# Kernel tuning notes

Hardware: AMD Instinct MI355X
Metric: run time of the kernel (lower is better)

Reference implementation:

```python
import jax, jax.numpy as jnp
import numpy as np

EPS = 1e-6


def rms_norm(h, w):
    # T5-style: no mean subtraction, no bias; variance in fp32
    var = jnp.mean(jnp.square(h.astype(jnp.float32)), axis=-1, keepdims=True)
    h = h * jax.lax.rsqrt(var + EPS)
    return w * h


def split_heads(t, n_heads):
    b, n, d = t.shape
    return t.reshape(b, n, n_heads, d // n_heads).transpose(0, 2, 1, 3)  # [B,H,N,dk]


def unify_heads(t):
    b, h, n, dk = t.shape
    return t.transpose(0, 2, 1, 3).reshape(b, n, h * dk)


def attention(q_in, kv_in, bias, wq, wk, wv, wo, n_heads):
    q = split_heads(q_in @ wq, n_heads)   # [B,H,Nq,dk]
    k = split_heads(kv_in @ wk, n_heads)  # [B,H,Nk,dk]
    v = split_heads(kv_in @ wv, n_heads)
    scores = jnp.einsum('bhqd,bhkd->bhqk', q, k) + bias  # no 1/sqrt(dk) scaling (T5 style)
    w = jax.nn.softmax(scores.astype(jnp.float32), axis=-1).astype(scores.dtype)
    out = jnp.einsum('bhqk,bhkd->bhqd', w, v)
    return unify_heads(out) @ wo


def setup_inputs() -> dict:
    key = jax.random.key(0)
    ks = jax.random.split(key, 18)
    B, N, ENC_N, D, H, DFF = 4, 2048, 1024, 1024, 16, 4096
    s = 0.02
    inp = {
        'x': jax.random.normal(ks[0], (B, N, D), jnp.float32),
        'encoding': jax.random.normal(ks[1], (B, ENC_N, D), jnp.float32),
        'self_attention_position_bias': jax.random.normal(ks[2], (1, H, 1, N), jnp.float32),
        'enc_dec_attention_position_bias': jax.random.normal(ks[3], (1, H, N, ENC_N), jnp.float32),
        'wq_s': jax.random.normal(ks[4], (D, D), jnp.float32) * s,
        'wk_s': jax.random.normal(ks[5], (D, D), jnp.float32) * s,
        'wv_s': jax.random.normal(ks[6], (D, D), jnp.float32) * s,
        'wo_s': jax.random.normal(ks[7], (D, D), jnp.float32) * s,
        'wq_c': jax.random.normal(ks[8], (D, D), jnp.float32) * s,
        'wk_c': jax.random.normal(ks[9], (D, D), jnp.float32) * s,
        'wv_c': jax.random.normal(ks[10], (D, D), jnp.float32) * s,
        'wo_c': jax.random.normal(ks[11], (D, D), jnp.float32) * s,
        'ff1_w': jax.random.normal(ks[12], (D, DFF), jnp.float32) * s,
        'ff2_w': jax.random.normal(ks[13], (DFF, D), jnp.float32) * s,
        'norm1_w': jnp.ones((D,), jnp.float32),
        'norm2_w': jnp.ones((D,), jnp.float32),
        'norm3_w': jnp.ones((D,), jnp.float32),
    }
    return inp


def reference(x, encoding, self_attention_position_bias, enc_dec_attention_position_bias,
              wq_s, wk_s, wv_s, wo_s, wq_c, wk_c, wv_c, wo_c,
              ff1_w, ff2_w, norm1_w, norm2_w, norm3_w):
    n_heads = 16
    # --- self-attention (decoder: single query = last token) ---
    normed = rms_norm(x, norm1_w)
    q_in = normed[:, -1:, :]  # [B,1,D]
    attn_out = attention(q_in, normed, self_attention_position_bias,
                         wq_s, wk_s, wv_s, wo_s, n_heads)  # [B,1,D]
    x = x + attn_out  # broadcast over sequence, matching torch in-place broadcast
    # --- cross-attention ---
    normed = rms_norm(x, norm2_w)
    cross_out = attention(normed, encoding, enc_dec_attention_position_bias,
                          wq_c, wk_c, wv_c, wo_c, n_heads)  # [B,N,D]
    x = x + cross_out
    # --- MLP ---
    normed = rms_norm(x, norm3_w)
    mlp_out = jax.nn.relu(normed @ ff1_w) @ ff2_w
    return x + mlp_out
```

## Files before the change

### kernel.cpp

```cpp
#include <hip/hip_runtime.h>
#include <stdint.h>

typedef unsigned short bfu;
typedef __bf16 bf8v __attribute__((ext_vector_type(8)));
typedef unsigned short us8 __attribute__((ext_vector_type(8)));
typedef unsigned short us4 __attribute__((ext_vector_type(4)));
typedef float f4v __attribute__((ext_vector_type(4)));

__device__ __forceinline__ float bf2f(bfu u) {
    union { unsigned u; float f; } c; c.u = ((unsigned)u) << 16; return c.f;
}
__device__ __forceinline__ bfu f2bf(float f) {
    union { float f; unsigned u; } c; c.f = f;
    unsigned r = c.u + 0x7fffu + ((c.u >> 16) & 1u);
    return (bfu)(r >> 16);
}
__device__ __forceinline__ f4v mfma16(us8 a, us8 b, f4v c) {
    return __builtin_amdgcn_mfma_f32_16x16x32_bf16(
        __builtin_bit_cast(bf8v, a), __builtin_bit_cast(bf8v, b), c, 0, 0, 0);
}

template<int BM, int BN, int EPI>
__global__ __launch_bounds__(256) void gemm_bt(
    const bfu* __restrict__ A, const bfu* __restrict__ Bt,
    const float* __restrict__ resF, void* __restrict__ outP,
    int K, int lda, int ldb, int ldc,
    long long aZs, long long aBs, long long aHs,
    long long bZs, long long bBs, long long bHs,
    long long cZs, long long cBs, long long cHs,
    int bh0)
{
    constexpr int BK = 64;
    constexpr int WM = BM / 2, WN = BN / 2;
    constexpr int TM = WM / 16, TN = WN / 16;
    __shared__ __align__(16) bfu sA[BM * BK];
    __shared__ __align__(16) bfu sB[BN * BK];

    const int tid  = threadIdx.x;
    const int lane = tid & 63;
    const int wid  = tid >> 6;
    const int wr = wid >> 1, wc = wid & 1;

    const int z  = blockIdx.z;
    const int bh = bh0 + z;
    const int bb = bh >> 4, hh = bh & 15;
    const long long aOff = aZs * z + aBs * bb + aHs * hh;
    const long long bOff = bZs * z + bBs * bb + bHs * hh;
    const long long cOff = cZs * z + cBs * bb + cHs * hh;

    const int m0 = blockIdx.y * BM;
    const int n0 = blockIdx.x * BN;

    f4v acc[TM][TN];
    #pragma unroll
    for (int i = 0; i < TM; ++i)
        #pragma unroll
        for (int j = 0; j < TN; ++j)
            acc[i][j] = (f4v)0.0f;

    const bfu* gA = A + aOff + (long long)m0 * lda;
    const bfu* gB = Bt + bOff + (long long)n0 * ldb;
    const int rsub = tid >> 3;
    const int kb   = (tid & 7) * 8;

    for (int k0 = 0; k0 < K; k0 += BK) {
        us8 ra[BM / 32], rb[BN / 32];
        #pragma unroll
        for (int it = 0; it < BM / 32; ++it)
            ra[it] = *(const us8*)(gA + (long long)(it * 32 + rsub) * lda + k0 + kb);
        #pragma unroll
        for (int it = 0; it < BN / 32; ++it)
            rb[it] = *(const us8*)(gB + (long long)(it * 32 + rsub) * ldb + k0 + kb);

        __syncthreads();
        #pragma unroll
        for (int it = 0; it < BM / 32; ++it)
            *(us8*)&sA[(it * 32 + rsub) * BK + kb] = ra[it];
        #pragma unroll
        for (int it = 0; it < BN / 32; ++it)
            *(us8*)&sB[(it * 32 + rsub) * BK + kb] = rb[it];
        __syncthreads();

        #pragma unroll
        for (int kk = 0; kk < BK; kk += 32) {
            const int kro = kk + ((lane >> 4) << 3);
            us8 af[TM], bfr[TN];
            #pragma unroll
            for (int i = 0; i < TM; ++i)
                af[i] = *(const us8*)&sA[(wr * WM + i * 16 + (lane & 15)) * BK + kro];
            #pragma unroll
            for (int j = 0; j < TN; ++j)
                bfr[j] = *(const us8*)&sB[(wc * WN + j * 16 + (lane & 15)) * BK + kro];
            #pragma unroll
            for (int i = 0; i < TM; ++i)
                #pragma unroll
                for (int j = 0; j < TN; ++j)
                    acc[i][j] = mfma16(af[i], bfr[j], acc[i][j]);
        }
    }

    const int quad = lane >> 4;
    const int cn = lane & 15;
    #pragma unroll
    for (int i = 0; i < TM; ++i) {
        #pragma unroll
        for (int j = 0; j < TN; ++j) {
            const int col = n0 + wc * WN + j * 16 + cn;
            #pragma unroll
            for (int r = 0; r < 4; ++r) {
                const int row = m0 + wr * WM + i * 16 + quad * 4 + r;
                const long long idx = cOff + (long long)row * ldc + col;
                const float v = acc[i][j][r];
                if constexpr (EPI == 0) ((bfu*)outP)[idx] = f2bf(v);
                else if constexpr (EPI == 1) ((float*)outP)[idx] = resF[idx] + v;
                else ((bfu*)outP)[idx] = f2bf(fmaxf(v, 0.0f));
            }
        }
    }
}

#define SROW 1032
__global__ __launch_bounds__(256) void xattn(
    const bfu* __restrict__ q2,
    const bfu* __restrict__ k2,
    const bfu* __restrict__ v2t,
    const float* __restrict__ bias,
    bfu* __restrict__ O)
{
    __shared__ __align__(16) bfu S[32 * SROW];
    const int tid = threadIdx.x, lane = tid & 63, wid = tid >> 6;
    const int quad = lane >> 4, l16 = lane & 15;
    const int bh = blockIdx.y, b = bh >> 4, h = bh & 15;
    const int q0 = blockIdx.x * 32;

    const int prow = (wid & 1) * 16;
    const int kh0  = (wid >> 1) * 512;
    const bfu* qbase = q2 + ((long long)b * 2048 + q0 + prow) * 1024 + h * 64;
    const us8 af0 = *(const us8*)(qbase + (long long)l16 * 1024 + quad * 8);
    const us8 af1 = *(const us8*)(qbase + (long long)l16 * 1024 + 32 + quad * 8);
    const bfu* kbase = k2 + (long long)b * 1048576 + h * 64;
    #pragma unroll 4
    for (int t = 0; t < 32; ++t) {
        const int n0 = kh0 + t * 16;
        const bfu* kr = kbase + (long long)(n0 + l16) * 1024 + quad * 8;
        const us8 bf0 = *(const us8*)kr;
        const us8 bf1 = *(const us8*)(kr + 32);
        f4v acc = (f4v)0.0f;
        acc = mfma16(af0, bf0, acc);
        acc = mfma16(af1, bf1, acc);
        #pragma unroll
        for (int r = 0; r < 4; ++r)
            S[(prow + quad * 4 + r) * SROW + n0 + l16] = f2bf(acc[r]);
    }
    __syncthreads();

    const float* bb0 = bias + ((long long)h * 2048 + q0) * 1024;
    for (int rr = 0; rr < 8; ++rr) {
        const int row = wid * 8 + rr;
        bfu* sp = &S[row * SROW + lane * 16];
        const us8 s0 = *(const us8*)sp;
        const us8 s1 = *(const us8*)(sp + 8);
        const float* bp = bb0 + (long long)row * 1024 + lane * 16;
        f4v bv[4];
        #pragma unroll
        for (int j = 0; j < 4; ++j) bv[j] = *(const f4v*)(bp + j * 4);
        float v[16];
        #pragma unroll
        for (int j = 0; j < 8; ++j) v[j] = bf2f(s0[j]) + bv[j >> 2][j & 3];
        #pragma unroll
        for (int j = 0; j < 8; ++j) v[8 + j] = bf2f(s1[j]) + bv[2 + (j >> 2)][j & 3];
        float m = v[0];
        #pragma unroll
        for (int j = 1; j < 16; ++j) m = fmaxf(m, v[j]);
        #pragma unroll
        for (int o = 32; o; o >>= 1) m = fmaxf(m, __shfl_xor(m, o));
        float s = 0.f;
        #pragma unroll
        for (int j = 0; j < 16; ++j) { v[j] = __expf(v[j] - m); s += v[j]; }
        #pragma unroll
        for (int o = 32; o; o >>= 1) s += __shfl_xor(s, o);
        const float inv = 1.0f / s;
        us8 o0, o1;
        #pragma unroll
        for (int j = 0; j < 8; ++j) { o0[j] = f2bf(v[j] * inv); o1[j] = f2bf(v[8 + j] * inv); }
        *(us8*)sp = o0;
        *(us8*)(sp + 8) = o1;
    }
    __syncthreads();

    const int dc0 = (wid >> 1) * 32;
    const bfu* vb = v2t + (long long)bh * 65536;
    f4v acc[2];
    acc[0] = (f4v)0.0f; acc[1] = (f4v)0.0f;
    #pragma unroll 4
    for (int k0 = 0; k0 < 1024; k0 += 32) {
        const us8 pa = *(const us8*)&S[(prow + l16) * SROW + k0 + quad * 8];
        #pragma unroll
        for (int j = 0; j < 2; ++j) {
            const us8 vf = *(const us8*)(vb + (long long)(dc0 + j * 16 + l16) * 1024 + k0 + quad * 8);
            acc[j] = mfma16(pa, vf, acc[j]);
        }
    }
    bfu* ob = O + ((long long)b * 2048 + q0 + prow) * 1024 + h * 64 + dc0;
    #pragma unroll
    for (int j = 0; j < 2; ++j)
        #pragma unroll
        for (int r = 0; r < 4; ++r)
            ob[(long long)(quad * 4 + r) * 1024 + j * 16 + l16] = f2bf(acc[j][r]);
}

__global__ __launch_bounds__(256) void cvt_f2b(
    const float* __restrict__ in, bfu* __restrict__ out)
{
    const long long i = ((long long)blockIdx.x * 256 + threadIdx.x) * 4;
    f4v v = *(const f4v*)(in + i);
    us4 o;
    #pragma unroll
    for (int k = 0; k < 4; ++k) o[k] = f2bf(v[k]);
    *(us4*)(out + i) = o;
}

__global__ __launch_bounds__(256) void transpose_plain(
    const float* __restrict__ in, bfu* __restrict__ out, int R, int C)
{
    __shared__ bfu t[32][33];
    const int r0 = blockIdx.y * 32, c0 = blockIdx.x * 32;
    const int tx = threadIdx.x, ty = threadIdx.y;
    #pragma unroll
    for (int i = 0; i < 32; i += 8)
        t[ty + i][tx] = f2bf(in[(long long)(r0 + ty + i) * C + c0 + tx]);
    __syncthreads();
    #pragma unroll
    for (int i = 0; i < 32; i += 8)
        out[(long long)(c0 + ty + i) * R + r0 + tx] = t[tx][ty + i];
}

__global__ __launch_bounds__(256) void transpose_w8(
    const float* p0, const float* p1, const float* p2, const float* p3,
    const float* p4, const float* p5, const float* p6, const float* p7,
    bfu* __restrict__ out)
{
    __shared__ bfu t[32][33];
    const float* srcs[8] = {p0, p1, p2, p3, p4, p5, p6, p7};
    const int zz = blockIdx.z;
    const float* in = srcs[zz];
    bfu* o = out + (long long)zz * 1048576;
    const int r0 = blockIdx.y * 32, c0 = blockIdx.x * 32;
    const int tx = threadIdx.x, ty = threadIdx.y;
    #pragma unroll
    for (int i = 0; i < 32; i += 8)
        t[ty + i][tx] = f2bf(in[(long long)(r0 + ty + i) * 1024 + c0 + tx]);
    __syncthreads();
    #pragma unroll
    for (int i = 0; i < 32; i += 8)
        o[(long long)(c0 + ty + i) * 1024 + r0 + tx] = t[tx][ty + i];
}

__global__ __launch_bounds__(256) void transpose_v2(
    const bfu* __restrict__ v2, bfu* __restrict__ v2t)
{
    __shared__ bfu t[32][33];
    const int z = blockIdx.z, b = z >> 4, h = z & 15;
    const bfu* in = v2 + (long long)b * 1048576 + h * 64;
    bfu* o = v2t + (long long)z * 65536;
    const int c0 = blockIdx.x * 32, r0 = blockIdx.y * 32;
    const int tx = threadIdx.x, ty = threadIdx.y;
    #pragma unroll
    for (int i = 0; i < 32; i += 8)
        t[ty + i][tx] = in[(long long)(r0 + ty + i) * 1024 + c0 + tx];
    __syncthreads();
    #pragma unroll
    for (int i = 0; i < 32; i += 8)
        o[(long long)(c0 + ty + i) * 1024 + r0 + tx] = t[tx][ty + i];
}

__device__ __forceinline__ float blockSum4(float v, float* red) {
    const int lane = threadIdx.x & 63, wid = threadIdx.x >> 6;
    #pragma unroll
    for (int o = 32; o; o >>= 1) v += __shfl_xor(v, o);
    if (lane == 0) red[wid] = v;
    __syncthreads();
    return red[0] + red[1] + red[2] + red[3];
}

__global__ __launch_bounds__(256) void rmsnorm_f32k(
    const float* __restrict__ X, const float* __restrict__ w, bfu* __restrict__ O)
{
    __shared__ float red[4];
    const long long row = blockIdx.x;
    const int tid = threadIdx.x;
    f4v xv = *(const f4v*)(X + row * 1024 + tid * 4);
    float ss = 0.f;
    #pragma unroll
    for (int i = 0; i < 4; ++i) ss += xv[i] * xv[i];
    ss = blockSum4(ss, red);
    const float sc = rsqrtf(ss * (1.0f / 1024.0f) + 1e-6f);
    f4v wv = *(const f4v*)(w + tid * 4);
    us4 o4;
    #pragma unroll
    for (int i = 0; i < 4; ++i) o4[i] = f2bf(xv[i] * sc * wv[i]);
    *(us4*)(O + row * 1024 + tid * 4) = o4;
}

__global__ __launch_bounds__(256) void add_bcast_rmsnorm(
    const float* __restrict__ X, const float* __restrict__ attn,
    const float* __restrict__ w, float* __restrict__ X1, bfu* __restrict__ O)
{
    __shared__ float red[4];
    const long long row = blockIdx.x;
    const int b = (int)(row >> 11);
    const int tid = threadIdx.x;
    f4v xv = *(const f4v*)(X + row * 1024 + tid * 4);
    f4v av = *(const f4v*)(attn + b * 1024 + tid * 4);
    f4v v;
    float ss = 0.f;
    #pragma unroll
    for (int i = 0; i < 4; ++i) { v[i] = xv[i] + av[i]; ss += v[i] * v[i]; }
    *(f4v*)(X1 + row * 1024 + tid * 4) = v;
    ss = blockSum4(ss, red);
    const float sc = rsqrtf(ss * (1.0f / 1024.0f) + 1e-6f);
    f4v wv = *(const f4v*)(w + tid * 4);
    us4 o4;
    #pragma unroll
    for (int i = 0; i < 4; ++i) o4[i] = f2bf(v[i] * sc * wv[i]);
    *(us4*)(O + row * 1024 + tid * 4) = o4;
}

template<int OUTF>
__global__ __launch_bounds__(256) void vecmat(
    const bfu* __restrict__ A, const bfu* __restrict__ Bt, void* __restrict__ out,
    int K, int N, long long aStride, long long aBase)
{
    __shared__ float sa[1024];
    const int tid = threadIdx.x;
    const int b = blockIdx.y;
    const bfu* ar = A + aBase + (long long)b * aStride;
    for (int k = tid; k < K; k += 256) sa[k] = bf2f(ar[k]);
    __syncthreads();
    const int n = blockIdx.x * 256 + tid;
    if (n < N) {
        const bfu* wr = Bt + (long long)n * K;
        float s = 0.f;
        for (int k = 0; k < K; k += 8) {
            us8 wv = *(const us8*)(wr + k);
            #pragma unroll
            for (int j = 0; j < 8; ++j) s += sa[k + j] * bf2f(wv[j]);
        }
        if constexpr (OUTF) ((float*)out)[(long long)b * N + n] = s;
        else ((bfu*)out)[(long long)b * N + n] = f2bf(s);
    }
}

__global__ __launch_bounds__(256) void decode_attn(
    const bfu* __restrict__ qs, const bfu* __restrict__ Kt,
    const bfu* __restrict__ Vt, const float* __restrict__ bias,
    bfu* __restrict__ osmall)
{
    const int bh = blockIdx.x, b = bh >> 4, h = bh & 15;
    const int tid = threadIdx.x, lane = tid & 63, wid = tid >> 6;
    __shared__ float sq[64];
    __shared__ float sc[2048];
    __shared__ float red[4];
    __shared__ float po[4][64];
    if (tid < 64) sq[tid] = bf2f(qs[b * 1024 + h * 64 + tid]);
    __syncthreads();

    const bfu* Kb = Kt + (long long)b * 2048 * 1024 + h * 64;
    float lmax = -1e30f;
    for (int k = tid; k < 2048; k += 256) {
        const us8* kr = (const us8*)(Kb + (long long)k * 1024);
        float s = 0.f;
        #pragma unroll
        for (int j = 0; j < 8; ++j) {
            us8 kv = kr[j];
            #pragma unroll
            for (int t = 0; t < 8; ++t) s += sq[j * 8 + t] * bf2f(kv[t]);
        }
        s += bias[h * 2048 + k];
        sc[k] = s;
        lmax = fmaxf(lmax, s);
    }
    #pragma unroll
    for (int o = 32; o; o >>= 1) lmax = fmaxf(lmax, __shfl_xor(lmax, o));
    if (lane == 0) red[wid] = lmax;
    __syncthreads();
    const float m = fmaxf(fmaxf(red[0], red[1]), fmaxf(red[2], red[3]));
    __syncthreads();

    float lsum = 0.f;
    for (int k = tid; k < 2048; k += 256) {
        const float e = __expf(sc[k] - m);
        sc[k] = e; lsum += e;
    }
    #pragma unroll
    for (int o = 32; o; o >>= 1) lsum += __shfl_xor(lsum, o);
    if (lane == 0) red[wid] = lsum;
    __syncthreads();
    const float S = red[0] + red[1] + red[2] + red[3];

    const bfu* Vb = Vt + (long long)b * 2048 * 1024 + h * 64;
    const int d = tid & 63, ks = tid >> 6;
    float a = 0.f;
    for (int k = ks * 512; k < ks * 512 + 512; ++k)
        a += sc[k] * bf2f(Vb[(long long)k * 1024 + d]);
    po[ks][d] = a;
    __syncthreads();
    if (tid < 64) {
        const float r = (po[0][tid] + po[1][tid] + po[2][tid] + po[3][tid]) / S;
        osmall[b * 1024 + h * 64 + tid] = f2bf(r);
    }
}

extern "C" void kernel_launch(void* const* d_in, const int* in_sizes, int n_in,
                              void* d_out, int out_size, void* d_ws, size_t ws_size,
                              hipStream_t stream) {
    (void)in_sizes; (void)n_in; (void)out_size; (void)ws_size;
    const float* x     = (const float*)d_in[0];
    const float* enc   = (const float*)d_in[1];
    const float* sbias = (const float*)d_in[2];
    const float* cbias = (const float*)d_in[3];
    const float* wq_s  = (const float*)d_in[4];
    const float* wk_s  = (const float*)d_in[5];
    const float* wv_s  = (const float*)d_in[6];
    const float* wo_s  = (const float*)d_in[7];
    const float* wq_c  = (const float*)d_in[8];
    const float* wk_c  = (const float*)d_in[9];
    const float* wv_c  = (const float*)d_in[10];
    const float* wo_c  = (const float*)d_in[11];
    const float* ff1   = (const float*)d_in[12];
    const float* ff2   = (const float*)d_in[13];
    const float* n1w   = (const float*)d_in[14];
    const float* n2w   = (const float*)d_in[15];
    const float* n3w   = (const float*)d_in[16];
    float* out = (float*)d_out;

    char* ws = (char*)d_ws;
    size_t off = 0;
    auto alloc = [&](size_t bytes) -> void* {
        void* p = (void*)(ws + off);
        off += (bytes + 255) & ~(size_t)255;
        return p;
    };
    bfu*   normed = (bfu*)alloc((size_t)8192 * 1024 * 2);
    bfu*   bufA   = (bfu*)alloc((size_t)8192 * 1024 * 2);
    bfu*   bufB   = (bfu*)alloc((size_t)8192 * 1024 * 2);
    bfu*   k2b    = (bfu*)alloc((size_t)4096 * 1024 * 2);
    bfu*   v2b    = (bfu*)alloc((size_t)4096 * 1024 * 2);
    bfu*   v2t    = (bfu*)alloc((size_t)4096 * 1024 * 2);
    bfu*   encb   = (bfu*)alloc((size_t)4096 * 1024 * 2);
    float* x1f    = (float*)alloc((size_t)8192 * 1024 * 4);
    bfu*   wT     = (bfu*)alloc((size_t)8 * 1048576 * 2);
    bfu*   ff1T   = (bfu*)alloc((size_t)4096 * 1024 * 2);
    bfu*   ff2T   = (bfu*)alloc((size_t)4096 * 1024 * 2);
    bfu*   qsb    = (bfu*)alloc(4 * 1024 * 2);
    bfu*   osm    = (bfu*)alloc(4 * 1024 * 2);
    float* attnv  = (float*)alloc(4 * 1024 * 4);
    bfu*   H1     = bufA;

    const dim3 tb32(32, 8);

    cvt_f2b<<<dim3(4096), 256, 0, stream>>>(enc, encb);
    transpose_w8<<<dim3(32, 32, 8), tb32, 0, stream>>>(
        wq_s, wk_s, wv_s, wo_s, wq_c, wk_c, wv_c, wo_c, wT);
    transpose_plain<<<dim3(128, 32, 1), tb32, 0, stream>>>(ff1, ff1T, 1024, 4096);
    transpose_plain<<<dim3(32, 128, 1), tb32, 0, stream>>>(ff2, ff2T, 4096, 1024);

    rmsnorm_f32k<<<dim3(8192), 256, 0, stream>>>(x, n1w, normed);

    gemm_bt<128, 128, 0><<<dim3(8, 64, 1), 256, 0, stream>>>(
        normed, wT + 1 * 1048576, nullptr, bufA, 1024, 1024, 1024, 1024,
        0, 0, 0, 0, 0, 0, 0, 0, 0, 0);
    gemm_bt<128, 128, 0><<<dim3(8, 64, 1), 256, 0, stream>>>(
        normed, wT + 2 * 1048576, nullptr, bufB, 1024, 1024, 1024, 1024,
        0, 0, 0, 0, 0, 0, 0, 0, 0, 0);
    vecmat<0><<<dim3(4, 4), 256, 0, stream>>>(normed, wT + 0 * 1048576, qsb,
        1024, 1024, (long long)2048 * 1024, (long long)2047 * 1024);
    decode_attn<<<dim3(64), 256, 0, stream>>>(qsb, bufA, bufB, sbias, osm);
    vecmat<1><<<dim3(4, 4), 256, 0, stream>>>(osm, wT + 3 * 1048576, attnv,
        1024, 1024, 1024, 0);
    add_bcast_rmsnorm<<<dim3(8192), 256, 0, stream>>>(x, attnv, n2w, x1f, normed);

    gemm_bt<128, 128, 0><<<dim3(8, 64, 1), 256, 0, stream>>>(
        normed, wT + 4 * 1048576, nullptr, bufA, 1024, 1024, 1024, 1024,
        0, 0, 0, 0, 0, 0, 0, 0, 0, 0);
    gemm_bt<128, 128, 0><<<dim3(8, 32, 1), 256, 0, stream>>>(
        encb, wT + 5 * 1048576, nullptr, k2b, 1024, 1024, 1024, 1024,
        0, 0, 0, 0, 0, 0, 0, 0, 0, 0);
    gemm_bt<128, 128, 0><<<dim3(8, 32, 1), 256, 0, stream>>>(
        encb, wT + 6 * 1048576, nullptr, v2b, 1024, 1024, 1024, 1024,
        0, 0, 0, 0, 0, 0, 0, 0, 0, 0);
    transpose_v2<<<dim3(2, 32, 64), tb32, 0, stream>>>(v2b, v2t);

    xattn<<<dim3(64, 64), 256, 0, stream>>>(bufA, k2b, v2t, cbias, bufB);

    gemm_bt<128, 128, 1><<<dim3(8, 64, 1), 256, 0, stream>>>(
        bufB, wT + 7 * 1048576, x1f, x1f, 1024, 1024, 1024, 1024,
        0, 0, 0, 0, 0, 0, 0, 0, 0, 0);

    rmsnorm_f32k<<<dim3(8192), 256, 0, stream>>>(x1f, n3w, normed);
    for (int mc = 0; mc < 8192; mc += 4096) {
        gemm_bt<128, 128, 2><<<dim3(32, 32, 1), 256, 0, stream>>>(
            normed + (long long)mc * 1024, ff1T, nullptr, H1,
            1024, 1024, 1024, 4096,
            0, 0, 0, 0, 0, 0, 0, 0, 0, 0);
        gemm_bt<128, 128, 1><<<dim3(8, 32, 1), 256, 0, stream>>>(
            H1, ff2T, x1f + (long long)mc * 1024, out + (long long)mc * 1024,
            4096, 4096, 4096, 1024,
            0, 0, 0, 0, 0, 0, 0, 0, 0, 0);
    }
}
```

Baseline: 1.152 ms.

## Halve cross-attention query tile to 16 rows for higher occupancy

The cross-attention kernel now processes 16 query rows per block instead of 32, halving the shared-memory score buffer and doubling the grid. Each wave takes a quarter of the key range for QK^T and one 16-wide slice of the head dimension for PV. The launch bounds now request 4 blocks per CU, and the shared-memory row stride is padded differently. The aim is to raise occupancy so memory latency is hidden better. The cost is that K and V are reloaded from global memory twice as often.

```diff
diff --git a/kernel.cpp b/kernel.cpp
--- a/kernel.cpp
+++ b/kernel.cpp
@@ -119,28 +119,27 @@
     }
 }
 
-#define SROW 1032
-__global__ __launch_bounds__(256) void xattn(
+#define SROW 1036
+__global__ __launch_bounds__(256, 4) void xattn(
     const bfu* __restrict__ q2,
     const bfu* __restrict__ k2,
     const bfu* __restrict__ v2t,
     const float* __restrict__ bias,
     bfu* __restrict__ O)
 {
-    __shared__ __align__(16) bfu S[32 * SROW];
+    __shared__ __align__(16) bfu S[16 * SROW];
     const int tid = threadIdx.x, lane = tid & 63, wid = tid >> 6;
     const int quad = lane >> 4, l16 = lane & 15;
     const int bh = blockIdx.y, b = bh >> 4, h = bh & 15;
-    const int q0 = blockIdx.x * 32;
-
-    const int prow = (wid & 1) * 16;
-    const int kh0  = (wid >> 1) * 512;
-    const bfu* qbase = q2 + ((long long)b * 2048 + q0 + prow) * 1024 + h * 64;
+    const int q0 = blockIdx.x * 16;
+
+    const int kh0 = wid * 256;
+    const bfu* qbase = q2 + ((long long)b * 2048 + q0) * 1024 + h * 64;
     const us8 af0 = *(const us8*)(qbase + (long long)l16 * 1024 + quad * 8);
     const us8 af1 = *(const us8*)(qbase + (long long)l16 * 1024 + 32 + quad * 8);
     const bfu* kbase = k2 + (long long)b * 1048576 + h * 64;
     #pragma unroll 4
-    for (int t = 0; t < 32; ++t) {
+    for (int t = 0; t < 16; ++t) {
         const int n0 = kh0 + t * 16;
         const bfu* kr = kbase + (long long)(n0 + l16) * 1024 + quad * 8;
         const us8 bf0 = *(const us8*)kr;
@@ -150,13 +149,14 @@
         acc = mfma16(af1, bf1, acc);
         #pragma unroll
         for (int r = 0; r < 4; ++r)
-            S[(prow + quad * 4 + r) * SROW + n0 + l16] = f2bf(acc[r]);
+            S[(quad * 4 + r) * SROW + n0 + l16] = f2bf(acc[r]);
     }
     __syncthreads();
 
     const float* bb0 = bias + ((long long)h * 2048 + q0) * 1024;
-    for (int rr = 0; rr < 8; ++rr) {
-        const int row = wid * 8 + rr;
+    #pragma unroll 2
+    for (int rr = 0; rr < 4; ++rr) {
+        const int row = wid * 4 + rr;
         bfu* sp = &S[row * SROW + lane * 16];
         const us8 s0 = *(const us8*)sp;
         const us8 s1 = *(const us8*)(sp + 8);
@@ -188,25 +188,18 @@
     }
     __syncthreads();
 
-    const int dc0 = (wid >> 1) * 32;
-    const bfu* vb = v2t + (long long)bh * 65536;
-    f4v acc[2];
-    acc[0] = (f4v)0.0f; acc[1] = (f4v)0.0f;
+    const bfu* vb = v2t + (long long)bh * 65536 + (long long)(wid * 16 + l16) * 1024;
+    f4v acc3 = (f4v)0.0f;
     #pragma unroll 4
     for (int k0 = 0; k0 < 1024; k0 += 32) {
-        const us8 pa = *(const us8*)&S[(prow + l16) * SROW + k0 + quad * 8];
-        #pragma unroll
-        for (int j = 0; j < 2; ++j) {
-            const us8 vf = *(const us8*)(vb + (long long)(dc0 + j * 16 + l16) * 1024 + k0 + quad * 8);
-            acc[j] = mfma16(pa, vf, acc[j]);
-        }
-    }
-    bfu* ob = O + ((long long)b * 2048 + q0 + prow) * 1024 + h * 64 + dc0;
-    #pragma unroll
-    for (int j = 0; j < 2; ++j)
-        #pragma unroll
-        for (int r = 0; r < 4; ++r)
-            ob[(long long)(quad * 4 + r) * 1024 + j * 16 + l16] = f2bf(acc[j][r]);
+        const us8 pa = *(const us8*)&S[l16 * SROW + k0 + quad * 8];
+        const us8 vf = *(const us8*)(vb + k0 + quad * 8);
+        acc3 = mfma16(pa, vf, acc3);
+    }
+    bfu* ob = O + ((long long)b * 2048 + q0) * 1024 + h * 64 + wid * 16;
+    #pragma unroll
+    for (int r = 0; r < 4; ++r)
+        ob[(long long)(quad * 4 + r) * 1024 + l16] = f2bf(acc3[r]);
 }
 
 __global__ __launch_bounds__(256) void cvt_f2b(
@@ -491,7 +484,7 @@
         0, 0, 0, 0, 0, 0, 0, 0, 0, 0);
     transpose_v2<<<dim3(2, 32, 64), tb32, 0, stream>>>(v2b, v2t);
 
-    xattn<<<dim3(64, 64), 256, 0, stream>>>(bufA, k2b, v2t, cbias, bufB);
+    xattn<<<dim3(128, 64), 256, 0, stream>>>(bufA, k2b, v2t, cbias, bufB);
 
     gemm_bt<128, 128, 1><<<dim3(8, 64, 1), 256, 0, stream>>>(
         bufB, wT + 7 * 1048576, x1f, x1f, 1024, 1024, 1024, 1024,
```

New measurement: 1.113 ms. -3.4%, faster.
